# Kernel tuning notes

Measured on AMD Instinct MI355X. Metric: run time of the kernel, lower is better.

## Reference

```python
import jax, jax.numpy as jnp
import numpy as np

B, S, M = 128, 4096, 20
LOG_2PI = float(np.log(2.0 * np.pi))


def setup_inputs() -> dict:
    key = jax.random.key(0)
    k1, k2, k3, k4, k5 = jax.random.split(key, 5)
    xs = jax.random.normal(k1, (B, S, 5), dtype=jnp.float32)
    logits_pred = jax.random.normal(k2, (B, S, M), dtype=jnp.float32)
    mus_pred = jax.random.normal(k3, (B, S, M, 2), dtype=jnp.float32)
    # sigmas are Cholesky entries (l00, l10, l11); diagonal must be positive.
    sigmas_pred = jax.random.uniform(k4, (B, S, M, 3), dtype=jnp.float32) + 0.1
    pen_pred = jax.random.uniform(k5, (B, S, 3), dtype=jnp.float32)
    return {"xs": xs, "logits_pred": logits_pred, "mus_pred": mus_pred,
            "sigmas_pred": sigmas_pred, "pen_pred": pen_pred}


def reference(xs, logits_pred, mus_pred, sigmas_pred, pen_pred):
    # split stroke-5 format: (dx_abs, dy_abs) + 3 pen states
    position_true = xs[..., :2]          # [B,S,2]
    pen_true = xs[..., 2:]               # [B,S,3]

    # relative positions: roll by 1 along seq, first step prev = (0,0)
    position_prev = jnp.concatenate(
        [jnp.zeros_like(position_true[:, :1]), position_true[:, :-1]], axis=1)
    rel = position_true - position_prev  # [B,S,2]

    # closed-form 2D Gaussian log-density with lower-tri Cholesky
    # scale_tril entries (tril_indices(2,2) order): l00, l10, l11
    l00 = sigmas_pred[..., 0]            # [B,S,M]
    l10 = sigmas_pred[..., 1]
    l11 = sigmas_pred[..., 2]
    d = rel[:, :, None, :] - mus_pred    # [B,S,M,2]
    z0 = d[..., 0] / l00
    z1 = (d[..., 1] - l10 * z0) / l11
    comp_logp = (-0.5 * (z0 * z0 + z1 * z1)
                 - LOG_2PI - jnp.log(l00) - jnp.log(l11))  # [B,S,M]

    # mixture log-prob via logsumexp over components
    mix_logp = jax.nn.logsumexp(
        jax.nn.log_softmax(logits_pred, axis=-1) + comp_logp, axis=-1)  # [B,S]
    position_loss = -jnp.sum(mix_logp)

    # pen loss: faithful to source -> CrossEntropyLoss(input=pen_true, target=pen_pred)
    # (soft-target CE, mean reduction over B*S rows)
    logp = jax.nn.log_softmax(pen_true.reshape(-1, 3), axis=-1)
    pen_loss = jnp.mean(-jnp.sum(pen_pred.reshape(-1, 3) * logp, axis=-1))

    return position_loss + pen_loss
```

## Files before the change

### kernel.cpp

```cpp
#include <hip/hip_runtime.h>
#include <math.h>

#define BB 128
#define SS 4096
#define MM 20
#define NPOS (BB * SS)
#define POSB 128
#define THREADS 128
#define NBLOCKS (NPOS / POSB)

__device__ __forceinline__ float fast_rcp(float x) { return __builtin_amdgcn_rcpf(x); }

__global__ __launch_bounds__(THREADS, 1) void sketch_main(
    const float* __restrict__ xs,
    const float* __restrict__ logits,
    const float* __restrict__ mus,
    const float* __restrict__ sigmas,
    const float* __restrict__ pen_pred,
    float* __restrict__ partials)
{
    const float LOG_2PI = 1.8378770664093453f;
    __shared__ float sig_l[POSB * 61];
    __shared__ float mu_l [POSB * 41];
    __shared__ float lg_l [POSB * 21];

    const int t  = threadIdx.x;
    const int pb = blockIdx.x * POSB;
    const int p  = pb + t;
    const int s  = p & (SS - 1);

    const float4* gs = (const float4*)(sigmas + (size_t)pb * 60);
    const float4* gm = (const float4*)(mus    + (size_t)pb * 40);
    const float4* gl = (const float4*)(logits + (size_t)pb * 20);

    float4 vs[15], vm[10], vl[5];
#pragma unroll
    for (int i = 0; i < 15; ++i) vs[i] = gs[t + THREADS * i];
#pragma unroll
    for (int i = 0; i < 10; ++i) vm[i] = gm[t + THREADS * i];
#pragma unroll
    for (int i = 0; i < 5;  ++i) vl[i] = gl[t + THREADS * i];

    const float* xp = xs + (size_t)p * 5;
    float px = xp[0], py = xp[1];
    float pt0 = xp[2], pt1 = xp[3], pt2 = xp[4];
    float qx = 0.0f, qy = 0.0f;
    if (s != 0) { qx = xp[-5]; qy = xp[-4]; }
    const float* pp = pen_pred + (size_t)p * 3;
    float pp0 = pp[0], pp1 = pp[1], pp2 = pp[2];

    {
        int q = t / 15, r = t % 15;
#pragma unroll
        for (int i = 0; i < 15; ++i) {
            float* d = &sig_l[q * 61 + r * 4];
            d[0] = vs[i].x; d[1] = vs[i].y; d[2] = vs[i].z; d[3] = vs[i].w;
            q += 8; r += 8; if (r >= 15) { r -= 15; q += 1; }
        }
    }
    {
        int q = t / 10, r = t % 10;
#pragma unroll
        for (int i = 0; i < 10; ++i) {
            float* d = &mu_l[q * 41 + r * 4];
            d[0] = vm[i].x; d[1] = vm[i].y; d[2] = vm[i].z; d[3] = vm[i].w;
            q += 12; r += 8; if (r >= 10) { r -= 10; q += 1; }
        }
    }
    {
        int q = t / 5, r = t % 5;
#pragma unroll
        for (int i = 0; i < 5; ++i) {
            float* d = &lg_l[q * 21 + r * 4];
            d[0] = vl[i].x; d[1] = vl[i].y; d[2] = vl[i].z; d[3] = vl[i].w;
            q += 25; r += 3; if (r >= 5) { r -= 5; q += 1; }
        }
    }
    __syncthreads();

    const float rx = px - qx, ry = py - qy;
    const float* sl = &sig_l[t * 61];
    const float* ml = &mu_l [t * 41];
    const float* ll = &lg_l [t * 21];

    float a[20];
    float sel = 0.0f;
#pragma unroll
    for (int c = 0; c < MM; ++c) {
        float l00 = sl[3*c], l10 = sl[3*c+1], l11 = sl[3*c+2];
        float z0 = (rx - ml[2*c]) * fast_rcp(l00);
        float z1 = ((ry - ml[2*c+1]) - l10 * z0) * fast_rcp(l11);
        float lg = ll[c];
        a[c] = lg - 0.5f * (z0*z0 + z1*z1) - LOG_2PI - __logf(l00 * l11);
        sel += __expf(lg);
    }

    float mx = a[0];
#pragma unroll
    for (int c = 1; c < MM; ++c) mx = fmaxf(mx, a[c]);
    float se = 0.0f;
#pragma unroll
    for (int c = 0; c < MM; ++c) se += __expf(a[c] - mx);
    float mix_logp = (mx + __logf(se)) - __logf(sel);

    float pm = fmaxf(pt0, fmaxf(pt1, pt2));
    float lse3 = pm + __logf(__expf(pt0 - pm) + __expf(pt1 - pm) + __expf(pt2 - pm));
    float pen = -(pp0 * (pt0 - lse3) + pp1 * (pt1 - lse3) + pp2 * (pt2 - lse3));

    float val = -mix_logp + pen * (1.0f / (float)NPOS);

#pragma unroll
    for (int off = 32; off > 0; off >>= 1) val += __shfl_down(val, off, 64);
    __shared__ float red[THREADS / 64];
    int lane = t & 63, wid = t >> 6;
    if (lane == 0) red[wid] = val;
    __syncthreads();
    if (t == 0)
        partials[blockIdx.x] = red[0] + red[1];
}

__global__ __launch_bounds__(256) void sketch_reduce(
    const float* __restrict__ partials, float* __restrict__ out)
{
    float v = 0.0f;
    for (int i = threadIdx.x; i < NBLOCKS; i += 256) v += partials[i];
#pragma unroll
    for (int off = 32; off > 0; off >>= 1) v += __shfl_down(v, off, 64);
    __shared__ float red[4];
    int lane = threadIdx.x & 63, wid = threadIdx.x >> 6;
    if (lane == 0) red[wid] = v;
    __syncthreads();
    if (threadIdx.x == 0)
        out[0] = red[0] + red[1] + red[2] + red[3];
}

extern "C" void kernel_launch(void* const* d_in, const int* in_sizes, int n_in,
                              void* d_out, int out_size, void* d_ws, size_t ws_size,
                              hipStream_t stream) {
    const float* xs       = (const float*)d_in[0];
    const float* logits   = (const float*)d_in[1];
    const float* mus      = (const float*)d_in[2];
    const float* sigmas   = (const float*)d_in[3];
    const float* pen_pred = (const float*)d_in[4];
    float* out = (float*)d_out;
    float* partials = (float*)d_ws;

    sketch_main<<<NBLOCKS, THREADS, 0, stream>>>(xs, logits, mus, sigmas, pen_pred, partials);
    sketch_reduce<<<1, 256, 0, stream>>>(partials, out);
}
```

Measured before the change: 285.7 us.

## Make main kernel persistent with double-buffered LDS and register prefetch

```diff
diff --git a/kernel.cpp b/kernel.cpp
--- a/kernel.cpp
+++ b/kernel.cpp
@@ -5,9 +5,11 @@
 #define SS 4096
 #define MM 20
 #define NPOS (BB * SS)
-#define POSB 128
-#define THREADS 128
-#define NBLOCKS (NPOS / POSB)
+#define POSB 64
+#define THREADS 64
+#define GRID 512
+#define NBATCH (NPOS / POSB)
+#define NB_PER_BLOCK (NBATCH / GRID)
 
 __device__ __forceinline__ float fast_rcp(float x) { return __builtin_amdgcn_rcpf(x); }
 
@@ -20,118 +22,121 @@
     float* __restrict__ partials)
 {
     const float LOG_2PI = 1.8378770664093453f;
-    __shared__ float sig_l[POSB * 61];
-    __shared__ float mu_l [POSB * 41];
-    __shared__ float lg_l [POSB * 21];
+    __shared__ float sig_l[2][POSB * 61];
+    __shared__ float mu_l [2][POSB * 41];
+    __shared__ float lg_l [2][POSB * 21];
 
-    const int t  = threadIdx.x;
-    const int pb = blockIdx.x * POSB;
-    const int p  = pb + t;
-    const int s  = p & (SS - 1);
-
-    const float4* gs = (const float4*)(sigmas + (size_t)pb * 60);
-    const float4* gm = (const float4*)(mus    + (size_t)pb * 40);
-    const float4* gl = (const float4*)(logits + (size_t)pb * 20);
+    const int t = threadIdx.x;
+    const int base = blockIdx.x * NB_PER_BLOCK;
 
     float4 vs[15], vm[10], vl[5];
+    float nx0, nx1, nx2, nx3, nx4, nq0, nq1, np0, np1, np2;
+
+    auto issue_loads = [&](int batch) {
+        const int pb = batch * POSB;
+        const float4* gs = (const float4*)(sigmas + (size_t)pb * 60);
+        const float4* gm = (const float4*)(mus    + (size_t)pb * 40);
+        const float4* gl = (const float4*)(logits + (size_t)pb * 20);
 #pragma unroll
-    for (int i = 0; i < 15; ++i) vs[i] = gs[t + THREADS * i];
+        for (int i = 0; i < 15; ++i) vs[i] = gs[t + THREADS * i];
 #pragma unroll
-    for (int i = 0; i < 10; ++i) vm[i] = gm[t + THREADS * i];
+        for (int i = 0; i < 10; ++i) vm[i] = gm[t + THREADS * i];
 #pragma unroll
-    for (int i = 0; i < 5;  ++i) vl[i] = gl[t + THREADS * i];
+        for (int i = 0; i < 5;  ++i) vl[i] = gl[t + THREADS * i];
+        const int p = pb + t;
+        const float* xp = xs + (size_t)p * 5;
+        nx0 = xp[0]; nx1 = xp[1]; nx2 = xp[2]; nx3 = xp[3]; nx4 = xp[4];
+        nq0 = 0.0f; nq1 = 0.0f;
+        if ((p & (SS - 1)) != 0) { nq0 = xp[-5]; nq1 = xp[-4]; }
+        const float* pp = pen_pred + (size_t)p * 3;
+        np0 = pp[0]; np1 = pp[1]; np2 = pp[2];
+    };
 
-    const float* xp = xs + (size_t)p * 5;
-    float px = xp[0], py = xp[1];
-    float pt0 = xp[2], pt1 = xp[3], pt2 = xp[4];
-    float qx = 0.0f, qy = 0.0f;
-    if (s != 0) { qx = xp[-5]; qy = xp[-4]; }
-    const float* pp = pen_pred + (size_t)p * 3;
-    float pp0 = pp[0], pp1 = pp[1], pp2 = pp[2];
+    auto lds_write = [&](int buf) {
+        { int q = t / 15, r = t % 15;
+#pragma unroll
+          for (int i = 0; i < 15; ++i) {
+              float* d = &sig_l[buf][q * 61 + r * 4];
+              d[0] = vs[i].x; d[1] = vs[i].y; d[2] = vs[i].z; d[3] = vs[i].w;
+              q += 4; r += 4; if (r >= 15) { r -= 15; q += 1; } } }
+        { int q = t / 10, r = t % 10;
+#pragma unroll
+          for (int i = 0; i < 10; ++i) {
+              float* d = &mu_l[buf][q * 41 + r * 4];
+              d[0] = vm[i].x; d[1] = vm[i].y; d[2] = vm[i].z; d[3] = vm[i].w;
+              q += 6; r += 4; if (r >= 10) { r -= 10; q += 1; } } }
+        { int q = t / 5, r = t % 5;
+#pragma unroll
+          for (int i = 0; i < 5; ++i) {
+              float* d = &lg_l[buf][q * 21 + r * 4];
+              d[0] = vl[i].x; d[1] = vl[i].y; d[2] = vl[i].z; d[3] = vl[i].w;
+              q += 12; r += 4; if (r >= 5) { r -= 5; q += 1; } } }
+    };
 
-    {
-        int q = t / 15, r = t % 15;
+    issue_loads(base);
+    lds_write(0);
+
+    float acc = 0.0f;
+
+#pragma unroll 2
+    for (int j = 0; j < NB_PER_BLOCK; ++j) {
+        const float px = nx0, py = nx1, pt0 = nx2, pt1 = nx3, pt2 = nx4;
+        const float qx = nq0, qy = nq1;
+        const float pp0 = np0, pp1 = np1, pp2 = np2;
+
+        if (j + 1 < NB_PER_BLOCK) issue_loads(base + j + 1);
+
+        const float rx = px - qx, ry = py - qy;
+        const float* sl = &sig_l[j & 1][t * 61];
+        const float* ml = &mu_l [j & 1][t * 41];
+        const float* ll = &lg_l [j & 1][t * 21];
+
+        float a[20];
+        float sel = 0.0f;
 #pragma unroll
-        for (int i = 0; i < 15; ++i) {
-            float* d = &sig_l[q * 61 + r * 4];
-            d[0] = vs[i].x; d[1] = vs[i].y; d[2] = vs[i].z; d[3] = vs[i].w;
-            q += 8; r += 8; if (r >= 15) { r -= 15; q += 1; }
+        for (int c = 0; c < MM; ++c) {
+            float l00 = sl[3*c], l10 = sl[3*c+1], l11 = sl[3*c+2];
+            float z0 = (rx - ml[2*c]) * fast_rcp(l00);
+            float z1 = ((ry - ml[2*c+1]) - l10 * z0) * fast_rcp(l11);
+            float lg = ll[c];
+            a[c] = lg - 0.5f * (z0*z0 + z1*z1) - LOG_2PI - __logf(l00 * l11);
+            sel += __expf(lg);
         }
-    }
-    {
-        int q = t / 10, r = t % 10;
+        float mx = a[0];
 #pragma unroll
-        for (int i = 0; i < 10; ++i) {
-            float* d = &mu_l[q * 41 + r * 4];
-            d[0] = vm[i].x; d[1] = vm[i].y; d[2] = vm[i].z; d[3] = vm[i].w;
-            q += 12; r += 8; if (r >= 10) { r -= 10; q += 1; }
-        }
-    }
-    {
-        int q = t / 5, r = t % 5;
+        for (int c = 1; c < MM; ++c) mx = fmaxf(mx, a[c]);
+        float se = 0.0f;
 #pragma unroll
-        for (int i = 0; i < 5; ++i) {
-            float* d = &lg_l[q * 21 + r * 4];
-            d[0] = vl[i].x; d[1] = vl[i].y; d[2] = vl[i].z; d[3] = vl[i].w;
-            q += 25; r += 3; if (r >= 5) { r -= 5; q += 1; }
-        }
-    }
-    __syncthreads();
+        for (int c = 0; c < MM; ++c) se += __expf(a[c] - mx);
+        float mix_logp = (mx + __logf(se)) - __logf(sel);
 
-    const float rx = px - qx, ry = py - qy;
-    const float* sl = &sig_l[t * 61];
-    const float* ml = &mu_l [t * 41];
-    const float* ll = &lg_l [t * 21];
+        float pm = fmaxf(pt0, fmaxf(pt1, pt2));
+        float lse3 = pm + __logf(__expf(pt0 - pm) + __expf(pt1 - pm) + __expf(pt2 - pm));
+        float pen = -(pp0 * (pt0 - lse3) + pp1 * (pt1 - lse3) + pp2 * (pt2 - lse3));
 
-    float a[20];
-    float sel = 0.0f;
-#pragma unroll
-    for (int c = 0; c < MM; ++c) {
-        float l00 = sl[3*c], l10 = sl[3*c+1], l11 = sl[3*c+2];
-        float z0 = (rx - ml[2*c]) * fast_rcp(l00);
-        float z1 = ((ry - ml[2*c+1]) - l10 * z0) * fast_rcp(l11);
-        float lg = ll[c];
-        a[c] = lg - 0.5f * (z0*z0 + z1*z1) - LOG_2PI - __logf(l00 * l11);
-        sel += __expf(lg);
+        acc += -mix_logp + pen * (1.0f / (float)NPOS);
+
+        if (j + 1 < NB_PER_BLOCK) lds_write((j + 1) & 1);
     }
 
-    float mx = a[0];
 #pragma unroll
-    for (int c = 1; c < MM; ++c) mx = fmaxf(mx, a[c]);
-    float se = 0.0f;
-#pragma unroll
-    for (int c = 0; c < MM; ++c) se += __expf(a[c] - mx);
-    float mix_logp = (mx + __logf(se)) - __logf(sel);
-
-    float pm = fmaxf(pt0, fmaxf(pt1, pt2));
-    float lse3 = pm + __logf(__expf(pt0 - pm) + __expf(pt1 - pm) + __expf(pt2 - pm));
-    float pen = -(pp0 * (pt0 - lse3) + pp1 * (pt1 - lse3) + pp2 * (pt2 - lse3));
-
-    float val = -mix_logp + pen * (1.0f / (float)NPOS);
-
-#pragma unroll
-    for (int off = 32; off > 0; off >>= 1) val += __shfl_down(val, off, 64);
-    __shared__ float red[THREADS / 64];
-    int lane = t & 63, wid = t >> 6;
-    if (lane == 0) red[wid] = val;
-    __syncthreads();
-    if (t == 0)
-        partials[blockIdx.x] = red[0] + red[1];
+    for (int off = 32; off > 0; off >>= 1) acc += __shfl_down(acc, off, 64);
+    if (t == 0) partials[blockIdx.x] = acc;
 }
 
 __global__ __launch_bounds__(256) void sketch_reduce(
     const float* __restrict__ partials, float* __restrict__ out)
 {
-    float v = 0.0f;
-    for (int i = threadIdx.x; i < NBLOCKS; i += 256) v += partials[i];
+    double v = 0.0;
+    for (int i = threadIdx.x; i < GRID; i += 256) v += (double)partials[i];
 #pragma unroll
     for (int off = 32; off > 0; off >>= 1) v += __shfl_down(v, off, 64);
-    __shared__ float red[4];
+    __shared__ double red[4];
     int lane = threadIdx.x & 63, wid = threadIdx.x >> 6;
     if (lane == 0) red[wid] = v;
     __syncthreads();
     if (threadIdx.x == 0)
-        out[0] = red[0] + red[1] + red[2] + red[3];
+        out[0] = (float)(red[0] + red[1] + red[2] + red[3]);
 }
 
 extern "C" void kernel_launch(void* const* d_in, const int* in_sizes, int n_in,
@@ -145,6 +150,6 @@
     float* out = (float*)d_out;
     float* partials = (float*)d_ws;
 
-    sketch_main<<<NBLOCKS, THREADS, 0, stream>>>(xs, logits, mus, sigmas, pen_pred, partials);
+    sketch_main<<<GRID, THREADS, 0, stream>>>(xs, logits, mus, sigmas, pen_pred, partials);
     sketch_reduce<<<1, 256, 0, stream>>>(partials, out);
 }
```

Result: no change. 288.5 us (+1.0%).
